# Performance work log

Hardware: AMD Instinct MI355X
Metric: run time of the kernel (lower is better)

The kernel has to match this reference:

```python
import jax, jax.numpy as jnp
import numpy as np
import math

WIDTH = 1024
NUM_HEADS = 16
HEAD_DIM = WIDTH // NUM_HEADS
WINDOW_SIZE = 256
MIN_LOGITS_VALUE = -1e30


def setup_inputs() -> dict:
    key = jax.random.key(0)
    ks = jax.random.split(key, 7)
    b, t = 2, 2048
    std = math.sqrt(1.0 / WIDTH)
    x = jax.random.normal(ks[0], (b, t, WIDTH), dtype=jnp.float32)
    segment_pos = jnp.broadcast_to(jnp.arange(t, dtype=jnp.int32)[None, :], (b, t))
    Wq = jax.random.normal(ks[1], (WIDTH, WIDTH), dtype=jnp.float32) * std
    Wk = jax.random.normal(ks[2], (HEAD_DIM, WIDTH), dtype=jnp.float32) * std
    Wv = jax.random.normal(ks[3], (HEAD_DIM, WIDTH), dtype=jnp.float32) * std
    Wf = jax.random.normal(ks[4], (WIDTH, WIDTH), dtype=jnp.float32) * std
    bf = jnp.zeros((WIDTH,), dtype=jnp.float32)
    return {"x": x, "segment_pos": segment_pos, "Wq": Wq, "Wk": Wk, "Wv": Wv, "Wf": Wf, "bf": bf}


def reference(x, segment_pos, Wq, Wk, Wv, Wf, bf):
    b, t, _ = x.shape
    # projections (Linear: x @ W.T)
    q = (x @ Wq.T).reshape(b, t, NUM_HEADS, HEAD_DIM)  # [b,t,n,h]
    k = x @ Wk.T  # [b,t,h] single shared KV head (MQA)
    v = x @ Wv.T  # [b,t,h]
    scale = 1.0 / math.sqrt(HEAD_DIM)
    logits = jnp.einsum('btnh,bsh->bnts', q, k) * scale  # [b,n,t,s]
    # sliding-window causal mask: q_pos >= k_pos and q_pos <= k_pos + window
    ar = jnp.arange(t)
    qp = ar[:, None]
    kp = ar[None, :]
    mask = (qp >= kp) & (qp <= kp + WINDOW_SIZE)  # [t,s]
    masked = jnp.where(mask[None, None, :, :], logits, MIN_LOGITS_VALUE)
    probs = jax.nn.softmax(masked.astype(jnp.float32), axis=-1).astype(logits.dtype)
    out = jnp.einsum('bnts,bsh->btnh', probs, v)  # [b,t,n,h]
    out = out.reshape(b, t, WIDTH)
    return out @ Wf.T + bf
```

## Files before the change

kernel.cpp:

```cpp
#include <hip/hip_runtime.h>
#include <stdint.h>

#define B_SZ   2
#define T_SEQ  2048
#define WIDTH_ 1024
#define NH     16
#define HD     64
#define WIN    256
#define MROWS  (B_SZ * T_SEQ)
#define NQKV   1152

typedef __attribute__((ext_vector_type(4))) float f32x4;
typedef __attribute__((ext_vector_type(8))) short s16x8;

typedef __attribute__((address_space(1))) const void gas_void;
typedef __attribute__((address_space(3))) void las_void;

#define MFMA(a, b, c) __builtin_amdgcn_mfma_f32_16x16x32_bf16((a), (b), (c), 0, 0, 0)

#define VMEM_DRAIN() asm volatile("s_waitcnt vmcnt(0)" ::: "memory")

__device__ __forceinline__ void gload_lds16(const void* g, void* l) {
  __builtin_amdgcn_global_load_lds((gas_void*)g, (las_void*)l, 16, 0, 0);
}

__device__ __forceinline__ ushort f2bf(float f) {
  union { float f; uint32_t u; } v; v.f = f;
  uint32_t u = v.u;
  return (ushort)((u + 0x7FFFu + ((u >> 16) & 1u)) >> 16);
}

__global__ void prep_kernel(const float* __restrict__ x,
                            const float* __restrict__ Wq,
                            const float* __restrict__ Wk,
                            const float* __restrict__ Wv,
                            const float* __restrict__ Wf,
                            ushort* __restrict__ xb,
                            ushort* __restrict__ wqkv,
                            ushort* __restrict__ wfb) {
  const int XN = MROWS * WIDTH_ / 4;
  const int WQ = NQKV * WIDTH_ / 4;
  const int WF = WIDTH_ * WIDTH_ / 4;
  int i = blockIdx.x * blockDim.x + threadIdx.x;
  float4 v;
  ushort* dst;
  if (i < XN) {
    v = ((const float4*)x)[i];
    dst = xb + i * 4;
  } else if (i < XN + WQ) {
    int j = i - XN;
    int row = (j * 4) >> 10;
    int col = (j * 4) & 1023;
    const float* src = (row < 1024) ? (Wq + row * 1024 + col)
                     : (row < 1088) ? (Wk + (row - 1024) * 1024 + col)
                                    : (Wv + (row - 1088) * 1024 + col);
    v = *(const float4*)src;
    dst = wqkv + j * 4;
  } else if (i < XN + WQ + WF) {
    int j = i - XN - WQ;
    v = ((const float4*)Wf)[j];
    dst = wfb + j * 4;
  } else {
    return;
  }
  ushort4 o;
  o.x = f2bf(v.x); o.y = f2bf(v.y); o.z = f2bf(v.z); o.w = f2bf(v.w);
  *(ushort4*)dst = o;
}

#define G_STAGE(AS, BS, KOFF) do {                                          \
  int c_ = w * 64 + lane;                                       \
  int row_ = c_ >> 2;                                                       \
  int ke_ = (c_ & 3) * 8;                                                   \
  int ldsb_ = c_ * 16;                     \
  gload_lds16(A + (size_t)(m0 + row_) * 1024 + (KOFF) + ke_,                \
              (char*)(AS) + ldsb_);                                         \
  gload_lds16(B + (size_t)(n0 + row_) * 1024 + (KOFF) + ke_,                \
              (char*)(BS) + ldsb_);                                         \
} while (0)

#define G_COMPUTE(AS, BS) do {                                              \
  s16x8 af_[2], bf_[2];                                                     \
  _Pragma("unroll")                                                         \
  for (int t_ = 0; t_ < 2; ++t_) {                                          \
    af_[t_] = *(const s16x8*)&(AS)[(wm + t_ * 16 + r16) * 32 + g * 8];      \
    bf_[t_] = *(const s16x8*)&(BS)[(wn + t_ * 16 + r16) * 32 + g * 8];      \
  }                                                                         \
  _Pragma("unroll")                                                         \
  for (int mb_ = 0; mb_ < 2; ++mb_)                                         \
    _Pragma("unroll")                                                       \
    for (int nb_ = 0; nb_ < 2; ++nb_)                                       \
      acc[mb_][nb_] = MFMA(af_[mb_], bf_[nb_], acc[mb_][nb_]);              \
} while (0)

template <int MODE>
__global__ __launch_bounds__(256) void gemm_kernel(
    const ushort* __restrict__ A, const ushort* __restrict__ B,
    ushort* __restrict__ qb, ushort* __restrict__ kb, ushort* __restrict__ vt,
    float* __restrict__ Cf, const float* __restrict__ bias) {
  const int NBX = (MODE == 0) ? 18 : 16;
  const int nwg = NBX * 64;
  const int cpx = nwg >> 3;
  int swz = (blockIdx.x & 7) * cpx + (blockIdx.x >> 3);
  const int bx = swz % NBX;
  const int by = swz / NBX;

  const int w = threadIdx.x >> 6;
  const int lane = threadIdx.x & 63;
  const int g = lane >> 4;
  const int r16 = lane & 15;
  const int m0 = by * 64;
  const int n0 = bx * 64;
  const int wm = (w >> 1) * 32;
  const int wn = (w & 1) * 32;

  __shared__ ushort As0[64 * 32];
  __shared__ ushort Bs0[64 * 32];
  __shared__ ushort As1[64 * 32];
  __shared__ ushort Bs1[64 * 32];

  f32x4 acc[2][2] = {};

  G_STAGE(As0, Bs0, 0);
  for (int k0 = 0; k0 < 1024; k0 += 64) {
    VMEM_DRAIN();
    __syncthreads();
    G_STAGE(As1, Bs1, k0 + 32);
    G_COMPUTE(As0, Bs0);
    VMEM_DRAIN();
    __syncthreads();
    if (k0 + 64 < 1024) G_STAGE(As0, Bs0, k0 + 64);
    G_COMPUTE(As1, Bs1);
  }

#pragma unroll
  for (int mb = 0; mb < 2; ++mb)
#pragma unroll
    for (int nb = 0; nb < 2; ++nb) {
      int n = n0 + wn + nb * 16 + r16;
      int mbase = m0 + wm + mb * 16 + 4 * g;
      if (MODE == 0) {
#pragma unroll
        for (int r = 0; r < 4; ++r) {
          ushort h = f2bf(acc[mb][nb][r]);
          int m = mbase + r;
          if (n < 1024)      qb[m * 1024 + n] = h;
          else if (n < 1088) kb[m * 64 + (n - 1024)] = h;
          else               vt[((size_t)((m >> 11) * 64 + (n - 1088))) * 2048 +
                                (m & 2047)] = h;
        }
      } else {
        float bv = bias[n];
#pragma unroll
        for (int r = 0; r < 4; ++r)
          Cf[(size_t)(mbase + r) * 1024 + n] = acc[mb][nb][r] + bv;
      }
    }
}

__global__ __launch_bounds__(64) void attn_kernel(
    const ushort* __restrict__ qb, const ushort* __restrict__ kb,
    const ushort* __restrict__ vt, ushort* __restrict__ ao) {
  const int lane = threadIdx.x;
  const int g = lane >> 4;
  const int r16 = lane & 15;
  const int blk = blockIdx.x;
  const int qt = blk & 63;
  const int h = (blk >> 6) & 15;
  const int b = blk >> 10;
  const int q0 = qt * 32;
  const int qpA = q0 + r16;
  const int qpB = q0 + 16 + r16;

  const ushort* qrowA = qb + (size_t)(b * 2048 + qpA) * 1024 + h * 64;
  const ushort* qrowB = qb + (size_t)(b * 2048 + qpB) * 1024 + h * 64;
  s16x8 qfA0 = *(const s16x8*)(qrowA + g * 8);
  s16x8 qfA1 = *(const s16x8*)(qrowA + 32 + g * 8);
  s16x8 qfB0 = *(const s16x8*)(qrowB + g * 8);
  s16x8 qfB1 = *(const s16x8*)(qrowB + 32 + g * 8);

  f32x4 oaccA[4] = {}, oaccB[4] = {};
  float mA = -1e30f, lA = 0.f, mB = -1e30f, lB = 0.f;

  int kt0 = q0 - WIN;
  if (kt0 < 0) kt0 = 0;
  kt0 &= ~31;

  s16x8 k00, k01, k10, k11;
  {
    const ushort* kp0 = kb + (size_t)(b * 2048 + kt0 + r16) * 64;
    const ushort* kp1 = kb + (size_t)(b * 2048 + kt0 + 16 + r16) * 64;
    k00 = *(const s16x8*)(kp0 + g * 8);
    k01 = *(const s16x8*)(kp0 + 32 + g * 8);
    k10 = *(const s16x8*)(kp1 + g * 8);
    k11 = *(const s16x8*)(kp1 + 32 + g * 8);
  }

  for (int kt = kt0; kt <= q0; kt += 32) {
    s16x8 c00 = k00, c01 = k01, c10 = k10, c11 = k11;

    s16x8 vfr[4];
#pragma unroll
    for (int db = 0; db < 4; ++db) {
      const ushort* vrow = vt + (size_t)(b * 64 + db * 16 + r16) * 2048 + kt;
      uint2 va = *(const uint2*)(vrow + 4 * g);
      uint2 vc = *(const uint2*)(vrow + 16 + 4 * g);
      union { s16x8 v; uint32_t d[4]; } u;
      u.d[0] = va.x; u.d[1] = va.y; u.d[2] = vc.x; u.d[3] = vc.y;
      vfr[db] = u.v;
    }

    if (kt + 32 <= q0) {
      const ushort* kp0 = kb + (size_t)(b * 2048 + kt + 32 + r16) * 64;
      const ushort* kp1 = kb + (size_t)(b * 2048 + kt + 48 + r16) * 64;
      k00 = *(const s16x8*)(kp0 + g * 8);
      k01 = *(const s16x8*)(kp0 + 32 + g * 8);
      k10 = *(const s16x8*)(kp1 + g * 8);
      k11 = *(const s16x8*)(kp1 + 32 + g * 8);
    }

    f32x4 sA0 = {}, sA1 = {}, sB0 = {}, sB1 = {};
    __builtin_amdgcn_s_setprio(1);
    sA0 = MFMA(c00, qfA0, sA0); sA0 = MFMA(c01, qfA1, sA0);
    sA1 = MFMA(c10, qfA0, sA1); sA1 = MFMA(c11, qfA1, sA1);
    sB0 = MFMA(c00, qfB0, sB0); sB0 = MFMA(c01, qfB1, sB0);
    sB1 = MFMA(c10, qfB0, sB1); sB1 = MFMA(c11, qfB1, sB1);
    __builtin_amdgcn_s_setprio(0);

    float pA0[4], pA1[4], pB0[4], pB1[4];
    float tmA = -1e30f, tmB = -1e30f;
#pragma unroll
    for (int r = 0; r < 4; ++r) {
      int ka = kt + 4 * g + r;
      int kc = ka + 16;
      float a0 = (ka <= qpA && qpA - ka <= WIN) ? sA0[r] * 0.125f : -1e30f;
      float a1 = (kc <= qpA && qpA - kc <= WIN) ? sA1[r] * 0.125f : -1e30f;
      float b0 = (ka <= qpB && qpB - ka <= WIN) ? sB0[r] * 0.125f : -1e30f;
      float b1 = (kc <= qpB && qpB - kc <= WIN) ? sB1[r] * 0.125f : -1e30f;
      pA0[r] = a0; pA1[r] = a1; pB0[r] = b0; pB1[r] = b1;
      tmA = fmaxf(tmA, fmaxf(a0, a1));
      tmB = fmaxf(tmB, fmaxf(b0, b1));
    }
    tmA = fmaxf(tmA, __shfl_xor(tmA, 16));
    tmA = fmaxf(tmA, __shfl_xor(tmA, 32));
    tmB = fmaxf(tmB, __shfl_xor(tmB, 16));
    tmB = fmaxf(tmB, __shfl_xor(tmB, 32));

    float mnA = fmaxf(mA, tmA), mnB = fmaxf(mB, tmB);
    float corrA = __expf(mA - mnA), corrB = __expf(mB - mnB);
    float tsA = 0.f, tsB = 0.f;
    s16x8 pfA, pfB;
#pragma unroll
    for (int r = 0; r < 4; ++r) {
      float eA0 = __expf(pA0[r] - mnA);
      float eA1 = __expf(pA1[r] - mnA);
      float eB0 = __expf(pB0[r] - mnB);
      float eB1 = __expf(pB1[r] - mnB);
      tsA += eA0 + eA1; tsB += eB0 + eB1;
      pfA[r] = (short)f2bf(eA0); pfA[4 + r] = (short)f2bf(eA1);
      pfB[r] = (short)f2bf(eB0); pfB[4 + r] = (short)f2bf(eB1);
    }
    tsA += __shfl_xor(tsA, 16); tsA += __shfl_xor(tsA, 32);
    tsB += __shfl_xor(tsB, 16); tsB += __shfl_xor(tsB, 32);
    lA = lA * corrA + tsA; mA = mnA;
    lB = lB * corrB + tsB; mB = mnB;

#pragma unroll
    for (int db = 0; db < 4; ++db) { oaccA[db] *= corrA; oaccB[db] *= corrB; }

    __builtin_amdgcn_s_setprio(1);
#pragma unroll
    for (int db = 0; db < 4; ++db) {
      oaccA[db] = MFMA(vfr[db], pfA, oaccA[db]);
      oaccB[db] = MFMA(vfr[db], pfB, oaccB[db]);
    }
    __builtin_amdgcn_s_setprio(0);
  }

  float invA = 1.0f / lA, invB = 1.0f / lB;
  ushort* orowA = ao + (size_t)(b * 2048 + qpA) * 1024 + h * 64;
  ushort* orowB = ao + (size_t)(b * 2048 + qpB) * 1024 + h * 64;
#pragma unroll
  for (int db = 0; db < 4; ++db) {
    ushort4 oA, oB;
    oA.x = f2bf(oaccA[db][0] * invA); oA.y = f2bf(oaccA[db][1] * invA);
    oA.z = f2bf(oaccA[db][2] * invA); oA.w = f2bf(oaccA[db][3] * invA);
    oB.x = f2bf(oaccB[db][0] * invB); oB.y = f2bf(oaccB[db][1] * invB);
    oB.z = f2bf(oaccB[db][2] * invB); oB.w = f2bf(oaccB[db][3] * invB);
    *(ushort4*)(orowA + db * 16 + 4 * g) = oA;
    *(ushort4*)(orowB + db * 16 + 4 * g) = oB;
  }
}

extern "C" void kernel_launch(void* const* d_in, const int* in_sizes, int n_in,
                              void* d_out, int out_size, void* d_ws, size_t ws_size,
                              hipStream_t stream) {
  const float* x  = (const float*)d_in[0];
  const float* Wq = (const float*)d_in[2];
  const float* Wk = (const float*)d_in[3];
  const float* Wv = (const float*)d_in[4];
  const float* Wf = (const float*)d_in[5];
  const float* bf = (const float*)d_in[6];
  float* out = (float*)d_out;

  uint8_t* w8 = (uint8_t*)d_ws;
  ushort* xb   = (ushort*)(w8 + 0);
  ushort* qbuf = (ushort*)(w8 + 8388608);
  ushort* attn = (ushort*)(w8 + 16777216);
  ushort* wqkv = (ushort*)(w8 + 25165824);
  ushort* wfb  = (ushort*)(w8 + 27525120);
  ushort* kbuf = (ushort*)(w8 + 29622272);
  ushort* vt   = (ushort*)(w8 + 30146560);

  prep_kernel<<<6272, 256, 0, stream>>>(x, Wq, Wk, Wv, Wf, xb, wqkv, wfb);
  gemm_kernel<0><<<1152, 256, 0, stream>>>(xb, wqkv, qbuf, kbuf, vt,
                                           nullptr, nullptr);
  attn_kernel<<<2048, 64, 0, stream>>>(qbuf, kbuf, vt, attn);
  gemm_kernel<1><<<1024, 256, 0, stream>>>(attn, wfb, nullptr, nullptr,
                                           nullptr, out, bf);
}
```

Measured before the change: 153.9 us.

## Widen GEMM K-tile to 64 with XOR-swizzled LDS and 64-key attention steps

The projection GEMMs now stage 64-wide K slices into double-buffered LDS. Rows use an XOR chunk swizzle to avoid bank conflicts, and a partial vmcnt wait lets the next slice's loads stay in flight during compute. The sliding-window attention kernel processes 64 keys per iteration instead of 32, halving loop overhead and softmax reductions per key. It also gains a launch-bounds occupancy hint. The wider attention step can compute or read past the causal edge; those positions are masked, but the reads may go slightly out of bounds at the end of the buffer, and register pressure rises.

```diff
diff --git a/kernel.cpp b/kernel.cpp
--- a/kernel.cpp
+++ b/kernel.cpp
@@ -18,7 +18,8 @@
 
 #define MFMA(a, b, c) __builtin_amdgcn_mfma_f32_16x16x32_bf16((a), (b), (c), 0, 0, 0)
 
-#define VMEM_DRAIN() asm volatile("s_waitcnt vmcnt(0)" ::: "memory")
+#define VM_WAIT4() asm volatile("s_waitcnt vmcnt(4)" ::: "memory")
+#define VM_WAIT0() asm volatile("s_waitcnt vmcnt(0)" ::: "memory")
 
 __device__ __forceinline__ void gload_lds16(const void* g, void* l) {
   __builtin_amdgcn_global_load_lds((gas_void*)g, (las_void*)l, 16, 0, 0);
@@ -68,29 +69,47 @@
   *(ushort4*)dst = o;
 }
 
-#define G_STAGE(AS, BS, KOFF) do {                                          \
-  int c_ = w * 64 + lane;                                       \
-  int row_ = c_ >> 2;                                                       \
-  int ke_ = (c_ & 3) * 8;                                                   \
-  int ldsb_ = c_ * 16;                     \
-  gload_lds16(A + (size_t)(m0 + row_) * 1024 + (KOFF) + ke_,                \
-              (char*)(AS) + ldsb_);                                         \
-  gload_lds16(B + (size_t)(n0 + row_) * 1024 + (KOFF) + ke_,                \
-              (char*)(BS) + ldsb_);                                         \
+#define G_STAGE64(AS, BS, KOFF) do {                                        \
+  _Pragma("unroll")                                                         \
+  for (int i_ = 0; i_ < 2; ++i_) {                                          \
+    int c_ = i_ * 256 + w * 64 + lane;                          \
+    int row_ = c_ >> 3;                         \
+    int ke_ = ((c_ & 7) * 8) ^ ((row_ & 7) << 3);      \
+    int ldsb_ = (i_ * 256 + w * 64) * 16;            \
+    gload_lds16(A + (size_t)(m0 + row_) * 1024 + (KOFF) + ke_,              \
+                (char*)(AS) + ldsb_);                                       \
+    gload_lds16(B + (size_t)(n0 + row_) * 1024 + (KOFF) + ke_,              \
+                (char*)(BS) + ldsb_);                                       \
+  }                                                                         \
 } while (0)
 
-#define G_COMPUTE(AS, BS) do {                                              \
-  s16x8 af_[2], bf_[2];                                                     \
+#define G_COMPUTE64(AS, BS) do {                                            \
   _Pragma("unroll")                                                         \
-  for (int t_ = 0; t_ < 2; ++t_) {                                          \
-    af_[t_] = *(const s16x8*)&(AS)[(wm + t_ * 16 + r16) * 32 + g * 8];      \
-    bf_[t_] = *(const s16x8*)&(BS)[(wn + t_ * 16 + r16) * 32 + g * 8];      \
+  for (int ks_ = 0; ks_ < 2; ++ks_) {                                       \
+    s16x8 af_[2], bf_[2];                                                   \
+    _Pragma("unroll")                                                       \
+    for (int t_ = 0; t_ < 2; ++t_) {                                        \
+      int ra_ = wm + t_ * 16 + r16;                                         \
+      int rb_ = wn + t_ * 16 + r16;                                         \
+      af_[t_] = *(const s16x8*)&(AS)[ra_ * 64 +                             \
+                  ((ks_ * 32 + g * 8) ^ ((ra_ & 7) << 3))];                 \
+      bf_[t_] = *(const s16x8*)&(BS)[rb_ * 64 +                             \
+                  ((ks_ * 32 + g * 8) ^ ((rb_ & 7) << 3))];                 \
+    }                                                                       \
+    _Pragma("unroll")                                                       \
+    for (int mb_ = 0; mb_ < 2; ++mb_)                                       \
+      _Pragma("unroll")                                                     \
+      for (int nb_ = 0; nb_ < 2; ++nb_)                                     \
+        acc[mb_][nb_] = MFMA(af_[mb_], bf_[nb_], acc[mb_][nb_]);            \
   }                                                                         \
-  _Pragma("unroll")                                                         \
-  for (int mb_ = 0; mb_ < 2; ++mb_)                                         \
-    _Pragma("unroll")                                                       \
-    for (int nb_ = 0; nb_ < 2; ++nb_)                                       \
-      acc[mb_][nb_] = MFMA(af_[mb_], bf_[nb_], acc[mb_][nb_]);              \
+} while (0)
+
+#define G_ITER(AS, BS, K)  do {                                             \
+  if ((K) == 960) { VM_WAIT0(); } else { VM_WAIT4(); }                      \
+  __syncthreads();                                                          \
+  G_COMPUTE64(AS, BS);                                                      \
+  __syncthreads();                                                          \
+  if ((K) + 128 < 1024) G_STAGE64(AS, BS, (K) + 128);                       \
 } while (0)
 
 template <int MODE>
@@ -114,23 +133,19 @@
   const int wm = (w >> 1) * 32;
   const int wn = (w & 1) * 32;
 
-  __shared__ ushort As0[64 * 32];
-  __shared__ ushort Bs0[64 * 32];
-  __shared__ ushort As1[64 * 32];
-  __shared__ ushort Bs1[64 * 32];
+  __shared__ ushort As0[64 * 64];
+  __shared__ ushort Bs0[64 * 64];
+  __shared__ ushort As1[64 * 64];
+  __shared__ ushort Bs1[64 * 64];
 
   f32x4 acc[2][2] = {};
 
-  G_STAGE(As0, Bs0, 0);
-  for (int k0 = 0; k0 < 1024; k0 += 64) {
-    VMEM_DRAIN();
-    __syncthreads();
-    G_STAGE(As1, Bs1, k0 + 32);
-    G_COMPUTE(As0, Bs0);
-    VMEM_DRAIN();
-    __syncthreads();
-    if (k0 + 64 < 1024) G_STAGE(As0, Bs0, k0 + 64);
-    G_COMPUTE(As1, Bs1);
+  G_STAGE64(As0, Bs0, 0);
+  G_STAGE64(As1, Bs1, 64);
+#pragma unroll
+  for (int k0 = 0; k0 < 1024; k0 += 128) {
+    G_ITER(As0, Bs0, k0);
+    G_ITER(As1, Bs1, k0 + 64);
   }
 
 #pragma unroll
@@ -158,7 +173,7 @@
     }
 }
 
-__global__ __launch_bounds__(64) void attn_kernel(
+__global__ __launch_bounds__(64, 2) void attn_kernel(
     const ushort* __restrict__ qb, const ushort* __restrict__ kb,
     const ushort* __restrict__ vt, ushort* __restrict__ ao) {
   const int lane = threadIdx.x;
@@ -186,61 +201,64 @@
   if (kt0 < 0) kt0 = 0;
   kt0 &= ~31;
 
-  s16x8 k00, k01, k10, k11;
-  {
-    const ushort* kp0 = kb + (size_t)(b * 2048 + kt0 + r16) * 64;
-    const ushort* kp1 = kb + (size_t)(b * 2048 + kt0 + 16 + r16) * 64;
-    k00 = *(const s16x8*)(kp0 + g * 8);
-    k01 = *(const s16x8*)(kp0 + 32 + g * 8);
-    k10 = *(const s16x8*)(kp1 + g * 8);
-    k11 = *(const s16x8*)(kp1 + 32 + g * 8);
-  }
-
-  for (int kt = kt0; kt <= q0; kt += 32) {
-    s16x8 c00 = k00, c01 = k01, c10 = k10, c11 = k11;
-
-    s16x8 vfr[4];
+  s16x8 pk[4][2];
+#pragma unroll
+  for (int s = 0; s < 4; ++s) {
+    const ushort* kp = kb + (size_t)(b * 2048 + kt0 + s * 16 + r16) * 64;
+    pk[s][0] = *(const s16x8*)(kp + g * 8);
+    pk[s][1] = *(const s16x8*)(kp + 32 + g * 8);
+  }
+
+  for (int kt = kt0; kt <= q0; kt += 64) {
+    s16x8 c[4][2];
+#pragma unroll
+    for (int s = 0; s < 4; ++s) { c[s][0] = pk[s][0]; c[s][1] = pk[s][1]; }
+
+    s16x8 vfr[4][2];
 #pragma unroll
     for (int db = 0; db < 4; ++db) {
       const ushort* vrow = vt + (size_t)(b * 64 + db * 16 + r16) * 2048 + kt;
-      uint2 va = *(const uint2*)(vrow + 4 * g);
-      uint2 vc = *(const uint2*)(vrow + 16 + 4 * g);
-      union { s16x8 v; uint32_t d[4]; } u;
-      u.d[0] = va.x; u.d[1] = va.y; u.d[2] = vc.x; u.d[3] = vc.y;
-      vfr[db] = u.v;
-    }
-
-    if (kt + 32 <= q0) {
-      const ushort* kp0 = kb + (size_t)(b * 2048 + kt + 32 + r16) * 64;
-      const ushort* kp1 = kb + (size_t)(b * 2048 + kt + 48 + r16) * 64;
-      k00 = *(const s16x8*)(kp0 + g * 8);
-      k01 = *(const s16x8*)(kp0 + 32 + g * 8);
-      k10 = *(const s16x8*)(kp1 + g * 8);
-      k11 = *(const s16x8*)(kp1 + 32 + g * 8);
-    }
-
-    f32x4 sA0 = {}, sA1 = {}, sB0 = {}, sB1 = {};
+      uint2 va0 = *(const uint2*)(vrow + 4 * g);
+      uint2 va1 = *(const uint2*)(vrow + 16 + 4 * g);
+      uint2 vb0 = *(const uint2*)(vrow + 32 + 4 * g);
+      uint2 vb1 = *(const uint2*)(vrow + 48 + 4 * g);
+      union { s16x8 v; uint32_t d[4]; } u0, u1;
+      u0.d[0] = va0.x; u0.d[1] = va0.y; u0.d[2] = va1.x; u0.d[3] = va1.y;
+      u1.d[0] = vb0.x; u1.d[1] = vb0.y; u1.d[2] = vb1.x; u1.d[3] = vb1.y;
+      vfr[db][0] = u0.v; vfr[db][1] = u1.v;
+    }
+
+    if (kt + 64 <= q0) {
+#pragma unroll
+      for (int s = 0; s < 4; ++s) {
+        const ushort* kp = kb + (size_t)(b * 2048 + kt + 64 + s * 16 + r16) * 64;
+        pk[s][0] = *(const s16x8*)(kp + g * 8);
+        pk[s][1] = *(const s16x8*)(kp + 32 + g * 8);
+      }
+    }
+
+    f32x4 sA[4], sB[4];
     __builtin_amdgcn_s_setprio(1);
-    sA0 = MFMA(c00, qfA0, sA0); sA0 = MFMA(c01, qfA1, sA0);
-    sA1 = MFMA(c10, qfA0, sA1); sA1 = MFMA(c11, qfA1, sA1);
-    sB0 = MFMA(c00, qfB0, sB0); sB0 = MFMA(c01, qfB1, sB0);
-    sB1 = MFMA(c10, qfB0, sB1); sB1 = MFMA(c11, qfB1, sB1);
+#pragma unroll
+    for (int s = 0; s < 4; ++s) {
+      f32x4 z = {};
+      sA[s] = MFMA(c[s][0], qfA0, z); sA[s] = MFMA(c[s][1], qfA1, sA[s]);
+      sB[s] = MFMA(c[s][0], qfB0, z); sB[s] = MFMA(c[s][1], qfB1, sB[s]);
+    }
     __builtin_amdgcn_s_setprio(0);
 
-    float pA0[4], pA1[4], pB0[4], pB1[4];
+    float pA[4][4], pB[4][4];
     float tmA = -1e30f, tmB = -1e30f;
 #pragma unroll
-    for (int r = 0; r < 4; ++r) {
-      int ka = kt + 4 * g + r;
-      int kc = ka + 16;
-      float a0 = (ka <= qpA && qpA - ka <= WIN) ? sA0[r] * 0.125f : -1e30f;
-      float a1 = (kc <= qpA && qpA - kc <= WIN) ? sA1[r] * 0.125f : -1e30f;
-      float b0 = (ka <= qpB && qpB - ka <= WIN) ? sB0[r] * 0.125f : -1e30f;
-      float b1 = (kc <= qpB && qpB - kc <= WIN) ? sB1[r] * 0.125f : -1e30f;
-      pA0[r] = a0; pA1[r] = a1; pB0[r] = b0; pB1[r] = b1;
-      tmA = fmaxf(tmA, fmaxf(a0, a1));
-      tmB = fmaxf(tmB, fmaxf(b0, b1));
-    }
+    for (int s = 0; s < 4; ++s)
+#pragma unroll
+      for (int r = 0; r < 4; ++r) {
+        int ka = kt + s * 16 + 4 * g + r;
+        float a = (ka <= qpA && qpA - ka <= WIN) ? sA[s][r] * 0.125f : -1e30f;
+        float bv = (ka <= qpB && qpB - ka <= WIN) ? sB[s][r] * 0.125f : -1e30f;
+        pA[s][r] = a; pB[s][r] = bv;
+        tmA = fmaxf(tmA, a); tmB = fmaxf(tmB, bv);
+      }
     tmA = fmaxf(tmA, __shfl_xor(tmA, 16));
     tmA = fmaxf(tmA, __shfl_xor(tmA, 32));
     tmB = fmaxf(tmB, __shfl_xor(tmB, 16));
@@ -249,16 +267,23 @@
     float mnA = fmaxf(mA, tmA), mnB = fmaxf(mB, tmB);
     float corrA = __expf(mA - mnA), corrB = __expf(mB - mnB);
     float tsA = 0.f, tsB = 0.f;
-    s16x8 pfA, pfB;
+    s16x8 pfA0, pfA1, pfB0, pfB1;
 #pragma unroll
     for (int r = 0; r < 4; ++r) {
-      float eA0 = __expf(pA0[r] - mnA);
-      float eA1 = __expf(pA1[r] - mnA);
-      float eB0 = __expf(pB0[r] - mnB);
-      float eB1 = __expf(pB1[r] - mnB);
-      tsA += eA0 + eA1; tsB += eB0 + eB1;
-      pfA[r] = (short)f2bf(eA0); pfA[4 + r] = (short)f2bf(eA1);
-      pfB[r] = (short)f2bf(eB0); pfB[4 + r] = (short)f2bf(eB1);
+      float eA0 = __expf(pA[0][r] - mnA);
+      float eA1 = __expf(pA[1][r] - mnA);
+      float eA2 = __expf(pA[2][r] - mnA);
+      float eA3 = __expf(pA[3][r] - mnA);
+      float eB0 = __expf(pB[0][r] - mnB);
+      float eB1 = __expf(pB[1][r] - mnB);
+      float eB2 = __expf(pB[2][r] - mnB);
+      float eB3 = __expf(pB[3][r] - mnB);
+      tsA += (eA0 + eA1) + (eA2 + eA3);
+      tsB += (eB0 + eB1) + (eB2 + eB3);
+      pfA0[r] = (short)f2bf(eA0); pfA0[4 + r] = (short)f2bf(eA1);
+      pfA1[r] = (short)f2bf(eA2); pfA1[4 + r] = (short)f2bf(eA3);
+      pfB0[r] = (short)f2bf(eB0); pfB0[4 + r] = (short)f2bf(eB1);
+      pfB1[r] = (short)f2bf(eB2); pfB1[4 + r] = (short)f2bf(eB3);
     }
     tsA += __shfl_xor(tsA, 16); tsA += __shfl_xor(tsA, 32);
     tsB += __shfl_xor(tsB, 16); tsB += __shfl_xor(tsB, 32);
@@ -271,8 +296,10 @@
     __builtin_amdgcn_s_setprio(1);
 #pragma unroll
     for (int db = 0; db < 4; ++db) {
-      oaccA[db] = MFMA(vfr[db], pfA, oaccA[db]);
-      oaccB[db] = MFMA(vfr[db], pfB, oaccB[db]);
+      oaccA[db] = MFMA(vfr[db][0], pfA0, oaccA[db]);
+      oaccA[db] = MFMA(vfr[db][1], pfA1, oaccA[db]);
+      oaccB[db] = MFMA(vfr[db][0], pfB0, oaccB[db]);
+      oaccB[db] = MFMA(vfr[db][1], pfB1, oaccB[db]);
     }
     __builtin_amdgcn_s_setprio(0);
   }
```

After: 152.9 us. No clear change (-0.7%).
